# Kernel tuning notes

Measured on AMD Instinct MI355X. Metric: run time of the kernel, lower is better.

The kernel has to match this reference:

```python
import jax, jax.numpy as jnp
import numpy as np

B, S, T = 32, 512, 512
SRC_SIZE, TGT_SIZE, OUT_SIZE, NUM_HEAD = 2048, 1024, 1024, 8
HEAD_DIM = OUT_SIZE // NUM_HEAD  # 128


def setup_inputs() -> dict:
    key = jax.random.key(0)
    ks = jax.random.split(key, 12)
    src = jax.random.normal(ks[0], (B, S, SRC_SIZE), dtype=jnp.float32)
    tgt = jax.random.normal(ks[1], (B, T, TGT_SIZE), dtype=jnp.float32)
    # binary float masks (1=valid, 0=pad); guarantee at least one valid src per row
    src_mask = (jax.random.uniform(ks[2], (B, S)) > 0.3).astype(jnp.float32)
    src_mask = src_mask.at[:, 0].set(1.0)
    tgt_mask = (jax.random.uniform(ks[3], (B, T)) > 0.3).astype(jnp.float32)
    tgt_mask = tgt_mask.at[:, 0].set(1.0)
    # FCNet in this repo is weight_norm(Linear) with no activation at drop=0 -> plain Linear
    def lin(k, out_f, in_f):
        return jax.random.normal(k, (out_f, in_f), dtype=jnp.float32) / np.sqrt(in_f)
    W_src = lin(ks[4], 2 * OUT_SIZE, SRC_SIZE)
    b_src = jnp.zeros((2 * OUT_SIZE,), jnp.float32)
    W_tgt = lin(ks[5], OUT_SIZE, TGT_SIZE)
    b_tgt = jnp.zeros((OUT_SIZE,), jnp.float32)
    W_out = lin(ks[6], OUT_SIZE, OUT_SIZE + TGT_SIZE)
    b_out = jnp.zeros((OUT_SIZE,), jnp.float32)
    return {"src": src, "tgt": tgt, "src_mask": src_mask, "tgt_mask": tgt_mask,
            "W_src": W_src, "b_src": b_src, "W_tgt": W_tgt, "b_tgt": b_tgt,
            "W_out": W_out, "b_out": b_out}


def reference(src, tgt, src_mask, tgt_mask, W_src, b_src, W_tgt, b_tgt, W_out, b_out):
    b, s, _ = src.shape
    t = tgt.shape[1]
    # projections (FCNet == Linear here)
    src_trans = jnp.einsum('bsf,of->bso', src, W_src) + b_src        # [B,S,2D]
    tgt_trans = jnp.einsum('btf,of->bto', tgt, W_tgt) + b_tgt        # [B,T,D]
    src_trans = src_trans * src_mask[:, :, None]
    tgt_trans = tgt_trans * tgt_mask[:, :, None]
    src_key, src_val = jnp.split(src_trans, 2, axis=2)               # each [B,S,D]
    # contiguous per-head chunks == reshape
    k = src_key.reshape(b, s, NUM_HEAD, HEAD_DIM)
    v = src_val.reshape(b, s, NUM_HEAD, HEAD_DIM)
    q = tgt_trans.reshape(b, t, NUM_HEAD, HEAD_DIM)
    scores = jnp.einsum('bthd,bshd->bhts', q, k) / np.sqrt(HEAD_DIM)  # [B,H,T,S]
    scores = jnp.where(src_mask[:, None, None, :] == 0, -jnp.inf, scores)
    attn = jax.nn.softmax(scores, axis=-1)
    tgt_update = jnp.einsum('bhts,bshd->bthd', attn, v).reshape(b, t, OUT_SIZE)
    cat_tgt = jnp.concatenate([tgt, tgt_update], axis=2)             # [B,T,TGT+D]
    return jnp.einsum('btf,of->bto', cat_tgt, W_out) + b_out         # [B,T,D]
```

## Files before the change

### kernel.cpp

```cpp
#include <hip/hip_runtime.h>

typedef __attribute__((ext_vector_type(4))) float f32x4;
typedef __attribute__((ext_vector_type(8))) short short8;
typedef unsigned short u16;

__device__ __forceinline__ u16 f2bf(float f) {
  unsigned int u = __float_as_uint(f);
  return (u16)((u + 0x7fffu + ((u >> 16) & 1u)) >> 16);
}

__device__ __forceinline__ void gload16(const void* g, void* l) {
  __builtin_amdgcn_global_load_lds((const __attribute__((address_space(1))) void*)g,
                                   (__attribute__((address_space(3))) void*)l, 16, 0, 0);
}

__global__ void cvt_f32_bf16(const float* __restrict__ in, u16* __restrict__ out, int n4) {
  int i = blockIdx.x * blockDim.x + threadIdx.x;
  int stride = gridDim.x * blockDim.x;
  for (; i < n4; i += stride) {
    float4 v = ((const float4*)in)[i];
    ushort4 o;
    o.x = f2bf(v.x); o.y = f2bf(v.y); o.z = f2bf(v.z); o.w = f2bf(v.w);
    ((ushort4*)out)[i] = o;
  }
}

__global__ void cvt_tgt_strided(const float* __restrict__ in, u16* __restrict__ cat, int n4) {
  int i = blockIdx.x * blockDim.x + threadIdx.x;
  int stride = gridDim.x * blockDim.x;
  for (; i < n4; i += stride) {
    int e = i * 4;
    int row = e >> 10;
    int c = e & 1023;
    float4 v = ((const float4*)in)[i];
    ushort4 o;
    o.x = f2bf(v.x); o.y = f2bf(v.y); o.z = f2bf(v.z); o.w = f2bf(v.w);
    *(ushort4*)(cat + (size_t)row * 2048 + c) = o;
  }
}

template <bool MASK, bool OUTBF, bool VSPLIT>
__global__ __launch_bounds__(512) void gemm256(const u16* __restrict__ A, int lda,
                                               const u16* __restrict__ W,
                                               const float* __restrict__ bias,
                                               const float* __restrict__ rowmask,
                                               void* __restrict__ Cout, int ldc,
                                               int nbn, int K,
                                               u16* __restrict__ vTout) {
  __shared__ __align__(16) u16 lds[2 * 32768];
  const int tid = threadIdx.x;
  const int lane = tid & 63;
  const int wid = tid >> 6;
  const int lr = lane & 15, lh = lane >> 4;
  const int wm = wid >> 2;
  const int wn = wid & 3;

  const int nwg = gridDim.x;
  const int cpx = nwg >> 3;
  const int bid = (blockIdx.x & 7) * cpx + (blockIdx.x >> 3);
  const int bm = bid / nbn;
  const int bn = bid - bm * nbn;

  const int srow = tid >> 3;
  const int scol = ((tid & 7) ^ (srow & 7)) << 3;
  const u16* As0 = A + (size_t)(bm * 256 + srow) * lda + scol;
  const u16* Ws0 = W + (size_t)(bn * 256 + srow) * K + scol;

  auto stageA = [&](int h, int t, int buf) {
    char* d = (char*)lds + buf * 65536 + h * 16384 + tid * 16;
    const u16* s = As0 + (size_t)(h * 128) * lda + t * 64;
    gload16(s, d);
    gload16(s + (size_t)64 * lda, d + 8192);
  };
  auto stageB = [&](int h, int t, int buf) {
    char* d = (char*)lds + buf * 65536 + 32768 + h * 16384 + tid * 16;
    const u16* s = Ws0 + (size_t)(h * 128) * K + t * 64;
    gload16(s, d);
    gload16(s + (size_t)64 * K, d + 8192);
  };

  const int key = (lr & 7) << 4;
  const int sb0 = ((0 + lh) << 4) ^ key;
  const int sb1 = ((4 + lh) << 4) ^ key;
  const int arow = (wm * 64 + lr) * 128;
  const int brow = 32768 + (wn * 32 + lr) * 128;

  f32x4 acc[8][4];
#pragma unroll
  for (int m = 0; m < 8; ++m)
#pragma unroll
    for (int n = 0; n < 4; ++n) acc[m][n] = (f32x4){0.f, 0.f, 0.f, 0.f};

  const int NT = K >> 6;

  stageA(0, 0, 0); stageB(0, 0, 0); stageB(1, 0, 0); stageA(1, 0, 0);
  asm volatile("s_waitcnt vmcnt(2)" ::: "memory");
  __builtin_amdgcn_s_barrier();
  __builtin_amdgcn_sched_barrier(0);

  short8 a[4][2], a2[4][2], b0[2][2], b1[2][2];
  {
    const char* Lb = (const char*)lds;
#pragma unroll
    for (int m = 0; m < 4; ++m) {
      a[m][0] = *(const short8*)(Lb + arow + m * 2048 + sb0);
      a[m][1] = *(const short8*)(Lb + arow + m * 2048 + sb1);
    }
#pragma unroll
    for (int n = 0; n < 2; ++n) {
      b0[n][0] = *(const short8*)(Lb + brow + n * 2048 + sb0);
      b0[n][1] = *(const short8*)(Lb + brow + n * 2048 + sb1);
    }
  }

  for (int t = 0; t < NT; ++t) {
    const int cur = t & 1, nxt = cur ^ 1;
    const char* Lb = (const char*)lds + cur * 65536;
    const char* Ln = (const char*)lds + nxt * 65536;
    const bool pf = (t + 1 < NT);

#pragma unroll
    for (int n = 0; n < 2; ++n) {
      b1[n][0] = *(const short8*)(Lb + brow + 16384 + n * 2048 + sb0);
      b1[n][1] = *(const short8*)(Lb + brow + 16384 + n * 2048 + sb1);
    }
    if (pf) { stageA(0, t + 1, nxt); stageB(0, t + 1, nxt); }
    asm volatile("s_waitcnt lgkmcnt(4)" ::: "memory");
    __builtin_amdgcn_sched_barrier(0);
    __builtin_amdgcn_s_setprio(1);
#pragma unroll
    for (int m = 0; m < 4; ++m)
#pragma unroll
      for (int n = 0; n < 2; ++n) {
        acc[m][n] = __builtin_amdgcn_mfma_f32_16x16x32_bf16(a[m][0], b0[n][0], acc[m][n], 0, 0, 0);
        acc[m][n] = __builtin_amdgcn_mfma_f32_16x16x32_bf16(a[m][1], b0[n][1], acc[m][n], 0, 0, 0);
      }
    __builtin_amdgcn_s_setprio(0);
    if (pf) { asm volatile("s_waitcnt vmcnt(4)" ::: "memory"); }
    else    { asm volatile("s_waitcnt vmcnt(0)" ::: "memory"); }
    __builtin_amdgcn_s_barrier();
    __builtin_amdgcn_sched_barrier(0);

#pragma unroll
    for (int m = 0; m < 4; ++m) {
      a2[m][0] = *(const short8*)(Lb + 16384 + arow + m * 2048 + sb0);
      a2[m][1] = *(const short8*)(Lb + 16384 + arow + m * 2048 + sb1);
    }
    if (pf) stageB(1, t + 1, nxt);
    asm volatile("s_waitcnt lgkmcnt(8)" ::: "memory");
    __builtin_amdgcn_sched_barrier(0);
    __builtin_amdgcn_s_setprio(1);
#pragma unroll
    for (int m = 0; m < 4; ++m)
#pragma unroll
      for (int n = 0; n < 2; ++n) {
        acc[m][2 + n] = __builtin_amdgcn_mfma_f32_16x16x32_bf16(a[m][0], b1[n][0], acc[m][2 + n], 0, 0, 0);
        acc[m][2 + n] = __builtin_amdgcn_mfma_f32_16x16x32_bf16(a[m][1], b1[n][1], acc[m][2 + n], 0, 0, 0);
      }
    __builtin_amdgcn_s_setprio(0);
    __builtin_amdgcn_s_barrier();
    __builtin_amdgcn_sched_barrier(0);

    if (pf) stageA(1, t + 1, nxt);
    asm volatile("s_waitcnt lgkmcnt(0)" ::: "memory");
    __builtin_amdgcn_sched_barrier(0);
    __builtin_amdgcn_s_setprio(1);
#pragma unroll
    for (int m = 0; m < 4; ++m)
#pragma unroll
      for (int n = 0; n < 2; ++n) {
        acc[4 + m][n] = __builtin_amdgcn_mfma_f32_16x16x32_bf16(a2[m][0], b0[n][0], acc[4 + m][n], 0, 0, 0);
        acc[4 + m][n] = __builtin_amdgcn_mfma_f32_16x16x32_bf16(a2[m][1], b0[n][1], acc[4 + m][n], 0, 0, 0);
      }
    __builtin_amdgcn_s_setprio(0);
    if (pf) { asm volatile("s_waitcnt vmcnt(4)" ::: "memory"); }
    else    { asm volatile("s_waitcnt vmcnt(0)" ::: "memory"); }
    __builtin_amdgcn_s_barrier();
    __builtin_amdgcn_sched_barrier(0);

    if (pf) {
#pragma unroll
      for (int m = 0; m < 4; ++m) {
        a[m][0] = *(const short8*)(Ln + arow + m * 2048 + sb0);
        a[m][1] = *(const short8*)(Ln + arow + m * 2048 + sb1);
      }
#pragma unroll
      for (int n = 0; n < 2; ++n) {
        b0[n][0] = *(const short8*)(Ln + brow + n * 2048 + sb0);
        b0[n][1] = *(const short8*)(Ln + brow + n * 2048 + sb1);
      }
    }
    __builtin_amdgcn_sched_barrier(0);
    __builtin_amdgcn_s_setprio(1);
#pragma unroll
    for (int m = 0; m < 4; ++m)
#pragma unroll
      for (int n = 0; n < 2; ++n) {
        acc[4 + m][2 + n] = __builtin_amdgcn_mfma_f32_16x16x32_bf16(a2[m][0], b1[n][0], acc[4 + m][2 + n], 0, 0, 0);
        acc[4 + m][2 + n] = __builtin_amdgcn_mfma_f32_16x16x32_bf16(a2[m][1], b1[n][1], acc[4 + m][2 + n], 0, 0, 0);
      }
    __builtin_amdgcn_s_setprio(0);
    if (pf) { asm volatile("s_waitcnt vmcnt(2)" ::: "memory"); }
    __builtin_amdgcn_s_barrier();
    __builtin_amdgcn_sched_barrier(0);
  }

  const int r0 = bm * 256 + wm * 64 + lh * 4;
  const int c0 = bn * 256 + wn * 32 + lr;

  if constexpr (VSPLIT) {
    if (bn * 256 >= 1024) {
#pragma unroll
      for (int mi = 0; mi < 8; ++mi) {
        const int row_base = r0 + (mi >> 2) * 128 + (mi & 3) * 16;
        const int b = row_base >> 9;
        const int s = row_base & 511;
        float mk[4];
#pragma unroll
        for (int i = 0; i < 4; ++i) mk[i] = rowmask[row_base + i];
#pragma unroll
        for (int ni = 0; ni < 4; ++ni) {
          const int col = c0 + (ni >> 1) * 128 + (ni & 1) * 16;
          const float bv = bias[col];
          const int vcol = col - 1024;
          u16* vp = vTout + ((size_t)(b * 8 + (vcol >> 7)) * 128 + (vcol & 127)) * 512 + s;
          ushort4 o;
          o.x = f2bf((acc[mi][ni][0] + bv) * mk[0]);
          o.y = f2bf((acc[mi][ni][1] + bv) * mk[1]);
          o.z = f2bf((acc[mi][ni][2] + bv) * mk[2]);
          o.w = f2bf((acc[mi][ni][3] + bv) * mk[3]);
          *(ushort4*)vp = o;
        }
      }
      return;
    }
  }

#pragma unroll
  for (int mi = 0; mi < 8; ++mi) {
    const int row_base = r0 + (mi >> 2) * 128 + (mi & 3) * 16;
#pragma unroll
    for (int i = 0; i < 4; ++i) {
      const int row = row_base + i;
      float msk = 1.f;
      if constexpr (MASK) msk = rowmask[row];
#pragma unroll
      for (int ni = 0; ni < 4; ++ni) {
        const int col = c0 + (ni >> 1) * 128 + (ni & 1) * 16;
        float v = (acc[mi][ni][i] + bias[col]) * msk;
        if constexpr (OUTBF)
          ((u16*)Cout)[(size_t)row * ldc + col] = f2bf(v);
        else
          ((float*)Cout)[(size_t)row * ldc + col] = v;
      }
    }
  }
}

__global__ __launch_bounds__(256) void attn_fwd(const u16* __restrict__ q,
                                                const u16* __restrict__ kbuf,
                                                const u16* __restrict__ vT,
                                                const float* __restrict__ smask,
                                                u16* __restrict__ cat) {
  __shared__ __align__(16) u16 lds[20480];
  u16* Ks = lds;
  u16* Vt = lds + 8192;
  u16* Ps = lds + 16384;
  const int tid = threadIdx.x;
  const int lane = tid & 63;
  const int w = tid >> 6;
  const int lr = lane & 15, lh = lane >> 4;
  const int bh = blockIdx.x & 255;
  const int qb = blockIdx.x >> 8;
  const int b = bh >> 3;
  const int h = bh & 7;
  const int t0 = qb * 64 + w * 16;
  const float SCALE = 0.08838834764831845f;

  const u16* kbase = kbuf + (size_t)(b * 512) * 1024 + h * 128;
  const u16* vbase = vT + (size_t)bh * 128 * 512;

  short8 qf[4];
  {
    const u16* qp = q + (size_t)(b * 512 + t0 + lr) * 1024 + h * 128 + lh * 8;
#pragma unroll
    for (int kc = 0; kc < 4; ++kc) qf[kc] = *(const short8*)(qp + kc * 32);
  }

  f32x4 o[8];
#pragma unroll
  for (int dt = 0; dt < 8; ++dt) o[dt] = (f32x4){0.f, 0.f, 0.f, 0.f};
  float m_run[4], l_run[4];
#pragma unroll
  for (int i = 0; i < 4; ++i) { m_run[i] = -1e30f; l_run[i] = 0.f; }

  for (int s0 = 0; s0 < 512; s0 += 64) {
    __syncthreads();
#pragma unroll
    for (int it = 0; it < 4; ++it) {
      int idx = it * 256 + tid;
      int kr = idx >> 4, ks = idx & 15;
      gload16(kbase + (size_t)(s0 + kr) * 1024 + ((ks ^ (kr & 7)) * 8), (char*)Ks + idx * 16);
      int vr = idx >> 3, vs = idx & 7;
      gload16(vbase + (size_t)vr * 512 + s0 + ((vs ^ (vr & 7)) * 8), (char*)Vt + idx * 16);
    }
    asm volatile("s_waitcnt vmcnt(0)" ::: "memory");
    __syncthreads();

    f32x4 sc[4];
#pragma unroll
    for (int st = 0; st < 4; ++st) {
      f32x4 c = (f32x4){0.f, 0.f, 0.f, 0.f};
      const int row = st * 16 + lr;
#pragma unroll
      for (int kc = 0; kc < 4; ++kc) {
        short8 kb = *(const short8*)((const char*)Ks + row * 256 +
                                     ((kc * 64 + lh * 16) ^ ((row & 7) << 4)));
        c = __builtin_amdgcn_mfma_f32_16x16x32_bf16(qf[kc], kb, c, 0, 0, 0);
      }
      sc[st] = c;
    }

    float cm[4];
#pragma unroll
    for (int st = 0; st < 4; ++st) cm[st] = smask[b * 512 + s0 + st * 16 + lr];

    float pv[4][4], mx[4];
#pragma unroll
    for (int i = 0; i < 4; ++i) mx[i] = -1e30f;
#pragma unroll
    for (int st = 0; st < 4; ++st)
#pragma unroll
      for (int i = 0; i < 4; ++i) {
        float v = (cm[st] != 0.f) ? sc[st][i] * SCALE : -1e30f;
        pv[st][i] = v;
        mx[i] = fmaxf(mx[i], v);
      }
#pragma unroll
    for (int off = 1; off < 16; off <<= 1)
#pragma unroll
      for (int i = 0; i < 4; ++i) mx[i] = fmaxf(mx[i], __shfl_xor(mx[i], off));

    float m_new[4], scl[4], rs[4];
#pragma unroll
    for (int i = 0; i < 4; ++i) {
      m_new[i] = fmaxf(m_run[i], mx[i]);
      scl[i] = __expf(m_run[i] - m_new[i]);
      rs[i] = 0.f;
    }
#pragma unroll
    for (int st = 0; st < 4; ++st)
#pragma unroll
      for (int i = 0; i < 4; ++i) {
        float p = (cm[st] != 0.f) ? __expf(pv[st][i] - m_new[i]) : 0.f;
        pv[st][i] = p;
        rs[i] += p;
      }
#pragma unroll
    for (int off = 1; off < 16; off <<= 1)
#pragma unroll
      for (int i = 0; i < 4; ++i) rs[i] += __shfl_xor(rs[i], off);
#pragma unroll
    for (int i = 0; i < 4; ++i) {
      l_run[i] = l_run[i] * scl[i] + rs[i];
      m_run[i] = m_new[i];
    }
#pragma unroll
    for (int dt = 0; dt < 8; ++dt)
#pragma unroll
      for (int i = 0; i < 4; ++i) o[dt][i] *= scl[i];

#pragma unroll
    for (int st = 0; st < 4; ++st)
#pragma unroll
      for (int i = 0; i < 4; ++i) {
        const int prow = lh * 4 + i;
        Ps[w * 1024 + prow * 64 + (((st * 2 + (lr >> 3)) ^ (prow & 7)) * 8) + (lr & 7)] =
            f2bf(pv[st][i]);
      }

    short8 pa[2];
#pragma unroll
    for (int s2 = 0; s2 < 2; ++s2)
      pa[s2] = *(const short8*)(Ps + w * 1024 + lr * 64 + (((s2 * 4 + lh) ^ (lr & 7)) * 8));
#pragma unroll
    for (int dt = 0; dt < 8; ++dt) {
#pragma unroll
      for (int s2 = 0; s2 < 2; ++s2) {
        const int row = dt * 16 + lr;
        short8 vb = *(const short8*)((const char*)Vt + row * 128 +
                                     ((s2 * 64 + lh * 16) ^ ((row & 7) << 4)));
        o[dt] = __builtin_amdgcn_mfma_f32_16x16x32_bf16(pa[s2], vb, o[dt], 0, 0, 0);
      }
    }
  }

  float inv[4];
#pragma unroll
  for (int i = 0; i < 4; ++i) inv[i] = 1.f / l_run[i];
  u16* outp = cat + (size_t)(b * 512 + t0 + lh * 4) * 2048 + 1024 + h * 128 + lr;
#pragma unroll
  for (int dt = 0; dt < 8; ++dt)
#pragma unroll
    for (int i = 0; i < 4; ++i)
      outp[(size_t)i * 2048 + dt * 16] = f2bf(o[dt][i] * inv[i]);
}

extern "C" void kernel_launch(void* const* d_in, const int* in_sizes, int n_in,
                              void* d_out, int out_size, void* d_ws, size_t ws_size,
                              hipStream_t stream) {
  (void)in_sizes; (void)n_in; (void)out_size; (void)ws_size;
  const float* src      = (const float*)d_in[0];
  const float* tgt      = (const float*)d_in[1];
  const float* src_mask = (const float*)d_in[2];
  const float* tgt_mask = (const float*)d_in[3];
  const float* W_src    = (const float*)d_in[4];
  const float* b_src    = (const float*)d_in[5];
  const float* W_tgt    = (const float*)d_in[6];
  const float* b_tgt    = (const float*)d_in[7];
  const float* W_out    = (const float*)d_in[8];
  const float* b_out    = (const float*)d_in[9];

  char* ws = (char*)d_ws;
  u16* catb = (u16*)(ws);
  u16* kbuf = (u16*)(ws + 67108864);
  u16* vTb  = (u16*)(ws + 100663296);
  u16* qbuf = (u16*)(ws + 134217728);
  u16* wsrc = (u16*)(ws + 167772160);
  u16* wtgt = (u16*)(ws + 176160768);
  u16* wout = (u16*)(ws + 178257920);

  cvt_f32_bf16<<<2048, 256, 0, stream>>>(src, catb, 16384 * 2048 / 4);
  cvt_f32_bf16<<<1024, 256, 0, stream>>>(W_src, wsrc, 2048 * 2048 / 4);
  cvt_f32_bf16<<<256, 256, 0, stream>>>(W_tgt, wtgt, 1024 * 1024 / 4);
  cvt_f32_bf16<<<512, 256, 0, stream>>>(W_out, wout, 1024 * 2048 / 4);

  gemm256<true, true, true><<<512, 512, 0, stream>>>(catb, 2048, wsrc, b_src, src_mask,
                                                     kbuf, 1024, 8, 2048, vTb);

  cvt_tgt_strided<<<1024, 256, 0, stream>>>(tgt, catb, 16384 * 1024 / 4);

  gemm256<true, true, false><<<256, 512, 0, stream>>>(catb, 2048, wtgt, b_tgt, tgt_mask,
                                                      qbuf, 1024, 4, 1024, nullptr);

  attn_fwd<<<2048, 256, 0, stream>>>(qbuf, kbuf, vTb, src_mask, catb);

  gemm256<false, false, false><<<256, 512, 0, stream>>>(catb, 2048, wout, b_out, nullptr,
                                                        (float*)d_out, 1024, 4, 2048, nullptr);
}
```

Baseline: 391.5 us.

## Simplify GEMM main loop to one barrier per K-tile with full-tile prefetch

Restructures the double-buffered bf16 GEMM loop so each iteration loads its fragments from the current LDS buffer at the top, issues all four next-tile global-to-LDS stages at once, and synchronizes only once at the end with vmcnt(0). This removes the three intermediate workgroup barriers and staggered vmcnt waits of the finer-grained ping-pong schedule. In exchange, LDS fragment reads for the next tile are no longer overlapped with the last MFMA group, and the full vmcnt(0) wait may expose global load latency.

```diff
diff --git a/kernel.cpp b/kernel.cpp
--- a/kernel.cpp
+++ b/kernel.cpp
@@ -3,6 +3,8 @@
 typedef __attribute__((ext_vector_type(4))) float f32x4;
 typedef __attribute__((ext_vector_type(8))) short short8;
 typedef unsigned short u16;
+
+#define SB0() __builtin_amdgcn_sched_barrier(0)
 
 __device__ __forceinline__ u16 f2bf(float f) {
   unsigned int u = __float_as_uint(f);
@@ -94,13 +96,17 @@
   const int NT = K >> 6;
 
   stageA(0, 0, 0); stageB(0, 0, 0); stageB(1, 0, 0); stageA(1, 0, 0);
-  asm volatile("s_waitcnt vmcnt(2)" ::: "memory");
+  asm volatile("s_waitcnt vmcnt(0)" ::: "memory");
   __builtin_amdgcn_s_barrier();
-  __builtin_amdgcn_sched_barrier(0);
-
-  short8 a[4][2], a2[4][2], b0[2][2], b1[2][2];
-  {
-    const char* Lb = (const char*)lds;
+  SB0();
+
+  for (int t = 0; t < NT; ++t) {
+    const int cur = t & 1, nxt = cur ^ 1;
+    const char* Lb = (const char*)lds + cur * 65536;
+    const bool pf = (t + 1 < NT);
+
+    short8 a[4][2], a2[4][2], b0[2][2], b1[2][2];
+
 #pragma unroll
     for (int m = 0; m < 4; ++m) {
       a[m][0] = *(const short8*)(Lb + arow + m * 2048 + sb0);
@@ -111,22 +117,17 @@
       b0[n][0] = *(const short8*)(Lb + brow + n * 2048 + sb0);
       b0[n][1] = *(const short8*)(Lb + brow + n * 2048 + sb1);
     }
-  }
-
-  for (int t = 0; t < NT; ++t) {
-    const int cur = t & 1, nxt = cur ^ 1;
-    const char* Lb = (const char*)lds + cur * 65536;
-    const char* Ln = (const char*)lds + nxt * 65536;
-    const bool pf = (t + 1 < NT);
-
+    SB0();
+    if (pf) { stageA(0, t + 1, nxt); stageB(0, t + 1, nxt);
+              stageB(1, t + 1, nxt); stageA(1, t + 1, nxt); }
 #pragma unroll
     for (int n = 0; n < 2; ++n) {
       b1[n][0] = *(const short8*)(Lb + brow + 16384 + n * 2048 + sb0);
       b1[n][1] = *(const short8*)(Lb + brow + 16384 + n * 2048 + sb1);
     }
-    if (pf) { stageA(0, t + 1, nxt); stageB(0, t + 1, nxt); }
+    SB0();
     asm volatile("s_waitcnt lgkmcnt(4)" ::: "memory");
-    __builtin_amdgcn_sched_barrier(0);
+    SB0();
     __builtin_amdgcn_s_setprio(1);
 #pragma unroll
     for (int m = 0; m < 4; ++m)
@@ -136,19 +137,13 @@
         acc[m][n] = __builtin_amdgcn_mfma_f32_16x16x32_bf16(a[m][1], b0[n][1], acc[m][n], 0, 0, 0);
       }
     __builtin_amdgcn_s_setprio(0);
-    if (pf) { asm volatile("s_waitcnt vmcnt(4)" ::: "memory"); }
-    else    { asm volatile("s_waitcnt vmcnt(0)" ::: "memory"); }
-    __builtin_amdgcn_s_barrier();
-    __builtin_amdgcn_sched_barrier(0);
-
 #pragma unroll
     for (int m = 0; m < 4; ++m) {
       a2[m][0] = *(const short8*)(Lb + 16384 + arow + m * 2048 + sb0);
       a2[m][1] = *(const short8*)(Lb + 16384 + arow + m * 2048 + sb1);
     }
-    if (pf) stageB(1, t + 1, nxt);
     asm volatile("s_waitcnt lgkmcnt(8)" ::: "memory");
-    __builtin_amdgcn_sched_barrier(0);
+    SB0();
     __builtin_amdgcn_s_setprio(1);
 #pragma unroll
     for (int m = 0; m < 4; ++m)
@@ -158,12 +153,8 @@
         acc[m][2 + n] = __builtin_amdgcn_mfma_f32_16x16x32_bf16(a[m][1], b1[n][1], acc[m][2 + n], 0, 0, 0);
       }
     __builtin_amdgcn_s_setprio(0);
-    __builtin_amdgcn_s_barrier();
-    __builtin_amdgcn_sched_barrier(0);
-
-    if (pf) stageA(1, t + 1, nxt);
     asm volatile("s_waitcnt lgkmcnt(0)" ::: "memory");
-    __builtin_amdgcn_sched_barrier(0);
+    SB0();
     __builtin_amdgcn_s_setprio(1);
 #pragma unroll
     for (int m = 0; m < 4; ++m)
@@ -172,26 +163,6 @@
         acc[4 + m][n] = __builtin_amdgcn_mfma_f32_16x16x32_bf16(a2[m][0], b0[n][0], acc[4 + m][n], 0, 0, 0);
         acc[4 + m][n] = __builtin_amdgcn_mfma_f32_16x16x32_bf16(a2[m][1], b0[n][1], acc[4 + m][n], 0, 0, 0);
       }
-    __builtin_amdgcn_s_setprio(0);
-    if (pf) { asm volatile("s_waitcnt vmcnt(4)" ::: "memory"); }
-    else    { asm volatile("s_waitcnt vmcnt(0)" ::: "memory"); }
-    __builtin_amdgcn_s_barrier();
-    __builtin_amdgcn_sched_barrier(0);
-
-    if (pf) {
-#pragma unroll
-      for (int m = 0; m < 4; ++m) {
-        a[m][0] = *(const short8*)(Ln + arow + m * 2048 + sb0);
-        a[m][1] = *(const short8*)(Ln + arow + m * 2048 + sb1);
-      }
-#pragma unroll
-      for (int n = 0; n < 2; ++n) {
-        b0[n][0] = *(const short8*)(Ln + brow + n * 2048 + sb0);
-        b0[n][1] = *(const short8*)(Ln + brow + n * 2048 + sb1);
-      }
-    }
-    __builtin_amdgcn_sched_barrier(0);
-    __builtin_amdgcn_s_setprio(1);
 #pragma unroll
     for (int m = 0; m < 4; ++m)
 #pragma unroll
@@ -200,9 +171,10 @@
         acc[4 + m][2 + n] = __builtin_amdgcn_mfma_f32_16x16x32_bf16(a2[m][1], b1[n][1], acc[4 + m][2 + n], 0, 0, 0);
       }
     __builtin_amdgcn_s_setprio(0);
-    if (pf) { asm volatile("s_waitcnt vmcnt(2)" ::: "memory"); }
+    SB0();
+    asm volatile("s_waitcnt vmcnt(0)" ::: "memory");
     __builtin_amdgcn_s_barrier();
-    __builtin_amdgcn_sched_barrier(0);
+    SB0();
   }
 
   const int r0 = bm * 256 + wm * 64 + lh * 4;
```

Measured after the change: 384.2 us. About the same (-1.9%).
